# Kernel optimization log

Hardware: AMD Instinct MI355X
Metric: run time of the kernel (lower is better)

Reference implementation:

```python
import jax, jax.numpy as jnp
import numpy as np

B, T, C = 4, 2048, 1024
T_PAST = 2048


def setup_inputs() -> dict:
    key = jax.random.key(0)
    ks = jax.random.split(key, 9)
    s = 1.0 / np.sqrt(C)
    return {
        "x": jax.random.normal(ks[0], (B, T, C), dtype=jnp.float32),
        "past_k": jax.random.normal(ks[1], (B, T_PAST, C), dtype=jnp.float32),
        "past_v": jax.random.normal(ks[2], (B, T_PAST, C), dtype=jnp.float32),
        "Wq": jax.random.normal(ks[3], (C, C), dtype=jnp.float32) * s,
        "bq": jnp.zeros((C,), dtype=jnp.float32),
        "Wk": jax.random.normal(ks[4], (C, C), dtype=jnp.float32) * s,
        "bk": jnp.zeros((C,), dtype=jnp.float32),
        "Wv": jax.random.normal(ks[5], (C, C), dtype=jnp.float32) * s,
        "bv": jnp.zeros((C,), dtype=jnp.float32),
    }


def reference(x, past_k, past_v, Wq, bq, Wk, bk, Wv, bv):
    Bb, Tt, Cc = x.shape
    # nn.Linear: y = x @ W^T + b
    Q = jnp.einsum('btc,dc->btd', x, Wq) + bq
    K = jnp.einsum('btc,dc->btd', x, Wk) + bk
    V = jnp.einsum('btc,dc->btd', x, Wv) + bv
    K = jnp.concatenate([past_k, K], axis=1)
    V = jnp.concatenate([past_v, V], axis=1)
    T_total = K.shape[1]
    scores = jnp.einsum('btc,bsc->bts', Q, K) / jnp.sqrt(jnp.float32(Cc))
    # Faithful to torch.tril(ones(T, T_total)): allow j <= i (even across cache)
    mask = jnp.arange(T_total)[None, :] <= jnp.arange(Tt)[:, None]
    scores = jnp.where(mask[None, :, :], scores, -jnp.inf)
    weights = jax.nn.softmax(scores, axis=-1)
    out = jnp.einsum('bts,bsc->btc', weights, V)
    return (out, K, V)
```

## Files before the change

### kernel.cpp

```cpp
#include <hip/hip_runtime.h>


typedef __bf16 bf16x8 __attribute__((ext_vector_type(8)));
typedef float f32x4 __attribute__((ext_vector_type(4)));

#define BB   4
#define TQ   2048
#define CD   1024
#define TPAST 2048
#define TTOT 4096
#define MROWS (BB * TQ)
#define SSTRIDE_FALLBACK ((size_t)TTOT * CD * 2)
#define SLOTU 8192
#define WSLOT 12288

__device__ __forceinline__ unsigned short f32_to_bf16u(float f) {
  unsigned int u = __float_as_uint(f);
  u += 0x7FFFu + ((u >> 16) & 1u);
  return (unsigned short)(u >> 16);
}
__device__ __forceinline__ float bf16u_to_f32(unsigned short h) {
  unsigned int u = ((unsigned int)h) << 16;
  return __uint_as_float(u);
}
__device__ __forceinline__ unsigned int pack_bf16(float a, float b) {
  return (unsigned int)f32_to_bf16u(a) | ((unsigned int)f32_to_bf16u(b) << 16);
}

__device__ __forceinline__ void gload_lds16(const unsigned short* g,
                                            unsigned short* l) {
  __builtin_amdgcn_global_load_lds(
      (const __attribute__((address_space(1))) void*)g,
      (__attribute__((address_space(3))) void*)l, 16, 0, 0);
}

__device__ __forceinline__ const unsigned short* swz_src(
    const unsigned short* base, size_t rowStart, size_t ld,
    int part, int wv, int lane) {
  int row = part * 64 + wv * 16 + (lane >> 2);
  int gp = (lane & 3) ^ ((lane >> 2) & 3);
  return base + (rowStart + row) * ld + gp * 8;
}

struct StagePtrs { const unsigned short *a0, *a1, *b0, *b1; };

__device__ __forceinline__ void stage_step(StagePtrs& p, unsigned short* lds,
                                           int stOff, int wv) {
  unsigned short* base = lds + stOff + wv * 512;
  gload_lds16(p.a0, base);
  gload_lds16(p.a1, base + 2048);
  gload_lds16(p.b0, base + 4096);
  gload_lds16(p.b1, base + 6144);
  p.a0 += 32; p.a1 += 32; p.b0 += 32; p.b1 += 32;
}

__device__ __forceinline__ void gemm_core_v2(
    StagePtrs p, unsigned short* lds, int NT,
    int wr, int wc, int lane, int wv, f32x4 acc[4][4]) {
  const int gph8 = (((lane >> 4) ^ (lane & 3))) * 8;
  const int aRd = (wr * 64 + (lane & 15)) * 32 + gph8;
  const int bRd = 4096 + (wc * 64 + (lane & 15)) * 32 + gph8;
  stage_step(p, lds, 0, wv);
  stage_step(p, lds, SLOTU, wv);
  int stOff = 2 * SLOTU;
  int rdOff = 0;
  for (int t = 0; t < NT; ++t) {
    if (t + 2 < NT) {
      stage_step(p, lds, stOff, wv);
      stOff = (stOff == 2 * SLOTU) ? 0 : stOff + SLOTU;
    }
    const int rem = NT - 1 - t;
    if (rem >= 2)      asm volatile("s_waitcnt vmcnt(8)" ::: "memory");
    else if (rem == 1) asm volatile("s_waitcnt vmcnt(4)" ::: "memory");
    else               asm volatile("s_waitcnt vmcnt(0)" ::: "memory");
    asm volatile("s_barrier" ::: "memory");
    bf16x8 af[4], bg[4];
#pragma unroll
    for (int i = 0; i < 4; ++i)
      af[i] = *(const bf16x8*)&lds[rdOff + aRd + i * 512];
#pragma unroll
    for (int i = 0; i < 4; ++i)
      bg[i] = *(const bf16x8*)&lds[rdOff + bRd + i * 512];
    asm volatile("s_waitcnt lgkmcnt(0)" ::: "memory");
    __builtin_amdgcn_sched_barrier(0);
    asm volatile("s_barrier" ::: "memory");
    __builtin_amdgcn_s_setprio(1);
#pragma unroll
    for (int mi = 0; mi < 4; ++mi)
#pragma unroll
      for (int ni = 0; ni < 4; ++ni)
        acc[mi][ni] = __builtin_amdgcn_mfma_f32_16x16x32_bf16(
            af[mi], bg[ni], acc[mi][ni], 0, 0, 0);
    __builtin_amdgcn_s_setprio(0);
    rdOff = (rdOff == 2 * SLOTU) ? 0 : rdOff + SLOTU;
  }
}

struct StageW { const unsigned short *a0, *a1, *b0, *b1, *b2, *b3; };

__device__ __forceinline__ void stage_w(StageW& p, unsigned short* lds,
                                        int stOff, int wv) {
  unsigned short* base = lds + stOff + wv * 512;
  gload_lds16(p.a0, base);
  gload_lds16(p.a1, base + 2048);
  gload_lds16(p.b0, base + 4096);
  gload_lds16(p.b1, base + 6144);
  gload_lds16(p.b2, base + 8192);
  gload_lds16(p.b3, base + 10240);
  p.a0 += 32; p.a1 += 32; p.b0 += 32; p.b1 += 32; p.b2 += 32; p.b3 += 32;
}

__device__ __forceinline__ void gemm_core_w(
    StageW p, unsigned short* lds, int NT,
    int wr, int wc, int lane, int wv, f32x4 acc[4][8]) {
  const int gph8 = (((lane >> 4) ^ (lane & 3))) * 8;
  const int aRd = (wr * 64 + (lane & 15)) * 32 + gph8;
  const int bRd = 4096 + (wc * 128 + (lane & 15)) * 32 + gph8;
  stage_w(p, lds, 0, wv);
  int stOff = WSLOT, rdOff = 0;
  for (int t = 0; t < NT; ++t) {
    if (t + 1 < NT) {
      stage_w(p, lds, stOff, wv);
      stOff ^= WSLOT;
    }
    if (t + 1 < NT) asm volatile("s_waitcnt vmcnt(6)" ::: "memory");
    else            asm volatile("s_waitcnt vmcnt(0)" ::: "memory");
    asm volatile("s_barrier" ::: "memory");
    bf16x8 af[4], bg[8];
#pragma unroll
    for (int i = 0; i < 4; ++i)
      af[i] = *(const bf16x8*)&lds[rdOff + aRd + i * 512];
#pragma unroll
    for (int i = 0; i < 8; ++i)
      bg[i] = *(const bf16x8*)&lds[rdOff + bRd + i * 512];
    asm volatile("s_waitcnt lgkmcnt(0)" ::: "memory");
    __builtin_amdgcn_sched_barrier(0);
    asm volatile("s_barrier" ::: "memory");
    __builtin_amdgcn_s_setprio(1);
#pragma unroll
    for (int mi = 0; mi < 4; ++mi)
#pragma unroll
      for (int ni = 0; ni < 8; ++ni)
        acc[mi][ni] = __builtin_amdgcn_mfma_f32_16x16x32_bf16(
            af[mi], bg[ni], acc[mi][ni], 0, 0, 0);
    __builtin_amdgcn_s_setprio(0);
    rdOff ^= WSLOT;
  }
}

#define TP_PAD 134
#define VCT_BLOCKS 2048
#define R0_END 2097152
#define R1_END 2359296
#define R2_END 2621440
#define R3_END 2883584
#define R4_END 4980736
__global__ __launch_bounds__(256) void prep(
    const float* __restrict__ x, const float* __restrict__ wq,
    const float* __restrict__ wk, const float* __restrict__ wv,
    const float* __restrict__ pk, const float* __restrict__ pV,
    unsigned short* __restrict__ xb, unsigned short* __restrict__ wqb,
    unsigned short* __restrict__ wkb, unsigned short* __restrict__ wvb,
    unsigned short* __restrict__ kb,
    float* __restrict__ outV, unsigned short* __restrict__ VT,
    float* __restrict__ outKcopy) {
  const int tid = threadIdx.x;
  if (blockIdx.x < VCT_BLOCKS) {
    __shared__ unsigned short T[32 * TP_PAD];
    const int bid = blockIdx.x;
    const int s0 = (bid & 63) * 32, c0 = ((bid >> 6) & 7) * 128, b = bid >> 9;
    const int s = tid >> 3, i8 = tid & 7;
    const float* src = &pV[(size_t)(b * TPAST + s0 + s) * CD + c0];
    float* dst = &outV[(size_t)b * (TTOT * CD) + (size_t)(s0 + s) * CD + c0];
#pragma unroll
    for (int k = 0; k < 4; ++k) {
      int c = k * 32 + i8 * 4;
      float4 f = *(const float4*)&src[c];
      *(float4*)&dst[c] = f;
      *(unsigned int*)&T[s * TP_PAD + c]     = pack_bf16(f.x, f.y);
      *(unsigned int*)&T[s * TP_PAD + c + 2] = pack_bf16(f.z, f.w);
    }
    __syncthreads();
    const int c = tid >> 2, sq = tid & 3;
#pragma unroll
    for (int ii = 0; ii < 2; ++ii) {
      int cc = c + ii * 64;
      unsigned short tmp[8];
#pragma unroll
      for (int j = 0; j < 8; ++j) tmp[j] = T[(sq * 8 + j) * TP_PAD + cc];
      *(uint4*)&VT[(size_t)(b * CD + c0 + cc) * TPAST + s0 + sq * 8] = *(uint4*)tmp;
    }
    return;
  }
  int i = (blockIdx.x - VCT_BLOCKS) * 256 + tid;
  const float* src; unsigned short* dst; int off;
  bool isPk = false;
  if (i < R0_END)      { src = x;  dst = xb;  off = i; }
  else if (i < R1_END) { src = wq; dst = wqb; off = i - R0_END; }
  else if (i < R2_END) { src = wk; dst = wkb; off = i - R1_END; }
  else if (i < R3_END) { src = wv; dst = wvb; off = i - R2_END; }
  else                 { src = pk; dst = kb;  off = i - R3_END; isPk = true; }
  float4 f = ((const float4*)src)[off];
  uint2 o;
  o.x = pack_bf16(f.x, f.y);
  o.y = pack_bf16(f.z, f.w);
  ((uint2*)dst)[off] = o;
  if (isPk && outKcopy) {
    int b = off >> 19;
    int rem = off & 524287;
    ((float4*)outKcopy)[(size_t)b * 1048576 + rem] = f;
  }
}

__global__ __launch_bounds__(256) void copy_past_kernel(
    const float* __restrict__ src, float* __restrict__ dst) {
  int i = blockIdx.x * 256 + threadIdx.x;
  int b = i >> 19;
  int rem = i & 524287;
  ((float4*)dst)[(size_t)b * 1048576 + rem] = ((const float4*)src)[i];
}

__global__ __launch_bounds__(256, 2) void proj_qkv(
    const unsigned short* __restrict__ A,
    const unsigned short* __restrict__ Wq_,
    const unsigned short* __restrict__ Wv_,
    const unsigned short* __restrict__ Wk_,
    const float* __restrict__ bq_, const float* __restrict__ bv_,
    const float* __restrict__ bk_,
    unsigned short* __restrict__ outQ,
    float* __restrict__ outV, float* __restrict__ outK) {
  __shared__ unsigned short lds[2 * WSLOT];
  const int tm = blockIdx.x * 128;
  const int which = blockIdx.y >> 2;
  const int tn = (blockIdx.y & 3) * 256;
  const unsigned short* W = (which == 0) ? Wq_ : (which == 1) ? Wv_ : Wk_;
  const float* bias = (which == 0) ? bq_ : (which == 1) ? bv_ : bk_;
  const int tid = threadIdx.x, lane = tid & 63, wv = tid >> 6;
  const int wr = wv >> 1, wc = wv & 1;
  StageW p;
  p.a0 = swz_src(A, tm, CD, 0, wv, lane);
  p.a1 = swz_src(A, tm, CD, 1, wv, lane);
  p.b0 = swz_src(W, tn, CD, 0, wv, lane);
  p.b1 = swz_src(W, tn, CD, 1, wv, lane);
  p.b2 = swz_src(W, tn, CD, 2, wv, lane);
  p.b3 = swz_src(W, tn, CD, 3, wv, lane);
  f32x4 acc[4][8] = {};
  gemm_core_w(p, lds, CD / 32, wr, wc, lane, wv, acc);
  const int rsub = (lane >> 4) * 4, csub = lane & 15;
#pragma unroll
  for (int mi = 0; mi < 4; ++mi)
#pragma unroll
    for (int ni = 0; ni < 8; ++ni) {
      int gcn = tn + wc * 128 + ni * 16 + csub;
      float bvv = bias[gcn];
#pragma unroll
      for (int r = 0; r < 4; ++r) {
        int grw = tm + wr * 64 + mi * 16 + rsub + r;
        float v = acc[mi][ni][r] + bvv;
        if (which == 0) {
          outQ[(size_t)grw * CD + gcn] = f32_to_bf16u(v * 0.03125f);
        } else {
          int b = grw >> 11, t = grw & (TQ - 1);
          float* o = (which == 1) ? outV : outK;
          o[(size_t)b * (TTOT * CD) + (size_t)(TPAST + t) * CD + gcn] = v;
        }
      }
    }
}

__global__ __launch_bounds__(256, 3) void score_gemm(
    const unsigned short* __restrict__ Q,
    const unsigned short* __restrict__ KB,
    unsigned short* __restrict__ S16, size_t sstride,
    float* __restrict__ l_part) {
  const int t0 = blockIdx.x * 128, s0 = blockIdx.y * 128, b = blockIdx.z;
  if (s0 > t0) return;
  __shared__ unsigned short lds[3 * SLOTU];
  __shared__ float lpart[128][2];
  const int tid = threadIdx.x, lane = tid & 63, wv = tid >> 6;
  const int wr = wv >> 1, wc = wv & 1;
  StagePtrs p;
  p.a0 = swz_src(Q, (size_t)b * TQ + t0, CD, 0, wv, lane);
  p.a1 = swz_src(Q, (size_t)b * TQ + t0, CD, 1, wv, lane);
  p.b0 = swz_src(KB, (size_t)b * TPAST + s0, CD, 0, wv, lane);
  p.b1 = swz_src(KB, (size_t)b * TPAST + s0, CD, 1, wv, lane);
  f32x4 acc[4][4] = {};
  gemm_core_v2(p, lds, CD / 32, wr, wc, lane, wv, acc);
  const int rsub = (lane >> 4) * 4, csub = lane & 15;
  float rsum[4][4];
#pragma unroll
  for (int mi = 0; mi < 4; ++mi)
#pragma unroll
    for (int r = 0; r < 4; ++r) rsum[mi][r] = 0.f;
#pragma unroll
  for (int mi = 0; mi < 4; ++mi)
#pragma unroll
    for (int ni = 0; ni < 4; ++ni) {
      int gs = s0 + wc * 64 + ni * 16 + csub;
#pragma unroll
      for (int r = 0; r < 4; ++r) {
        int gt = t0 + wr * 64 + mi * 16 + rsub + r;
        float e = (gs <= gt) ? __expf(acc[mi][ni][r] - 16.f) : 0.f;
        unsigned short h = f32_to_bf16u(e);
        S16[(size_t)b * sstride + (size_t)gt * TPAST + gs] = h;
        rsum[mi][r] += bf16u_to_f32(h);
      }
    }
#pragma unroll
  for (int mi = 0; mi < 4; ++mi)
#pragma unroll
    for (int r = 0; r < 4; ++r) {
      float v = rsum[mi][r];
      v += __shfl_xor(v, 1);
      v += __shfl_xor(v, 2);
      v += __shfl_xor(v, 4);
      v += __shfl_xor(v, 8);
      rsum[mi][r] = v;
    }
  if ((lane & 15) == 0) {
#pragma unroll
    for (int mi = 0; mi < 4; ++mi)
#pragma unroll
      for (int r = 0; r < 4; ++r)
        lpart[wr * 64 + mi * 16 + rsub + r][wc] = rsum[mi][r];
  }
  __syncthreads();
  if (tid < 128)
    l_part[((size_t)b * TQ + t0 + tid) * 16 + (s0 >> 7)] =
        lpart[tid][0] + lpart[tid][1];
}

__global__ __launch_bounds__(256, 3) void pv_gemm(
    const unsigned short* __restrict__ Pb,
    const unsigned short* __restrict__ VT,
    float* __restrict__ O, size_t sstride,
    const float* __restrict__ l_part) {
  const int t0 = blockIdx.x * 128, c0 = blockIdx.y * 128, b = blockIdx.z;
  __shared__ unsigned short lds[3 * SLOTU];
  const int tid = threadIdx.x, lane = tid & 63, wv = tid >> 6;
  const int wr = wv >> 1, wc = wv & 1;
  StagePtrs p;
  p.a0 = swz_src(Pb + (size_t)b * sstride, t0, TPAST, 0, wv, lane);
  p.a1 = swz_src(Pb + (size_t)b * sstride, t0, TPAST, 1, wv, lane);
  p.b0 = swz_src(VT, (size_t)b * CD + c0, TPAST, 0, wv, lane);
  p.b1 = swz_src(VT, (size_t)b * CD + c0, TPAST, 1, wv, lane);
  f32x4 acc[4][4] = {};
  const int s_end = (t0 + 128 < TPAST) ? (t0 + 128) : TPAST;
  gemm_core_v2(p, lds, s_end / 32, wr, wc, lane, wv, acc);
  __syncthreads();
  float* linv = (float*)lds;
  if (tid < 128) {
    const float* lp = &l_part[((size_t)b * TQ + t0 + tid) * 16];
    float s = 0.f;
    const int nj = (t0 >> 7) + 1;
    for (int j = 0; j < nj; ++j) s += lp[j];
    linv[tid] = 1.0f / s;
  }
  __syncthreads();
  const int rsub = (lane >> 4) * 4, csub = lane & 15;
#pragma unroll
  for (int mi = 0; mi < 4; ++mi)
#pragma unroll
    for (int ni = 0; ni < 4; ++ni) {
      int gcn = c0 + wc * 64 + ni * 16 + csub;
#pragma unroll
      for (int r = 0; r < 4; ++r) {
        int lrow = wr * 64 + mi * 16 + rsub + r;
        int gt = t0 + lrow;
        O[(size_t)(b * TQ + gt) * CD + gcn] = acc[mi][ni][r] * linv[lrow];
      }
    }
}

extern "C" void kernel_launch(void* const* d_in, const int* in_sizes, int n_in,
                              void* d_out, int out_size, void* d_ws, size_t ws_size,
                              hipStream_t stream) {
  const float* x  = (const float*)d_in[0];
  const float* pk = (const float*)d_in[1];
  const float* pv = (const float*)d_in[2];
  const float* Wq = (const float*)d_in[3];
  const float* bq = (const float*)d_in[4];
  const float* Wk = (const float*)d_in[5];
  const float* bk = (const float*)d_in[6];
  const float* Wv = (const float*)d_in[7];
  const float* bv = (const float*)d_in[8];

  float* out  = (float*)d_out;
  float* outK = out + (size_t)BB * TQ * CD;
  float* outV = outK + (size_t)BB * TTOT * CD;

  unsigned short* xb  = (unsigned short*)d_ws;
  unsigned short* wqb = xb + (size_t)MROWS * CD;
  unsigned short* wkb = wqb + (size_t)CD * CD;
  unsigned short* wvb = wkb + (size_t)CD * CD;
  unsigned short* qb  = wvb + (size_t)CD * CD;
  unsigned short* vtb = qb + (size_t)MROWS * CD;
  unsigned short* kb  = vtb + (size_t)BB * CD * TPAST;
  unsigned short* wsEnd = kb + (size_t)BB * TPAST * CD;

  const size_t baseBytes = (size_t)((char*)wsEnd - (char*)d_ws);
  const size_t s16Bytes  = (size_t)BB * TQ * TPAST * 2;
  const size_t lpBytes   = (size_t)BB * TQ * 16 * 4;
  const bool fit = ws_size >= baseBytes + s16Bytes + lpBytes;

  unsigned short* S16;
  float* l_part;
  size_t sstride;
  if (fit) {
    S16 = wsEnd;
    l_part = (float*)(S16 + (size_t)BB * TQ * TPAST);
    sstride = (size_t)TQ * TPAST;
  } else {
    S16 = (unsigned short*)outK;
    l_part = (float*)wsEnd;
    sstride = SSTRIDE_FALLBACK;
  }

  prep<<<VCT_BLOCKS + R4_END / 256, 256, 0, stream>>>(
      x, Wq, Wk, Wv, pk, pv, xb, wqb, wkb, wvb, kb, outV, vtb,
      fit ? outK : nullptr);
  proj_qkv<<<dim3(MROWS / 128, 12), 256, 0, stream>>>(
      xb, wqb, wvb, wkb, bq, bv, bk, qb, outV, outK);
  score_gemm<<<dim3(TQ / 128, TPAST / 128, BB), 256, 0, stream>>>(
      qb, kb, S16, sstride, l_part);
  pv_gemm<<<dim3(TQ / 128, CD / 128, BB), 256, 0, stream>>>(
      S16, vtb, out, sstride, l_part);
  if (!fit)
    copy_past_kernel<<<BB * TPAST * CD / 4 / 256, 256, 0, stream>>>(pk, outK);
}
```

Before: 211.1 us.

## Retune GEMM pipelines, add nontemporal stores, reverse causal block order

In the projection GEMM, the LDS ring grows from double to triple buffering with a two-tile prefetch depth and matching vmcnt waits. In the score and PV GEMMs, prefetch depth drops to one tile over the three existing slots, which removes the second barrier and the lgkmcnt wait per iteration. Large fp32 output writes (V/K copies, projected K/V, attention output) become nontemporal stores so they do not pollute cache. Score and PV blocks are launched in reverse t order so the heaviest causal tiles are scheduled first. The larger LDS footprint in the projection kernel may reduce occupancy.

```diff
diff --git a/kernel.cpp b/kernel.cpp
--- a/kernel.cpp
+++ b/kernel.cpp
@@ -26,6 +26,11 @@
 __device__ __forceinline__ unsigned int pack_bf16(float a, float b) {
   return (unsigned int)f32_to_bf16u(a) | ((unsigned int)f32_to_bf16u(b) << 16);
 }
+__device__ __forceinline__ void nt_store4(float4 f, float* p) {
+  f32x4 v;
+  v[0] = f.x; v[1] = f.y; v[2] = f.z; v[3] = f.w;
+  __builtin_nontemporal_store(v, (f32x4*)p);
+}
 
 __device__ __forceinline__ void gload_lds16(const unsigned short* g,
                                             unsigned short* l) {
@@ -61,18 +66,16 @@
   const int aRd = (wr * 64 + (lane & 15)) * 32 + gph8;
   const int bRd = 4096 + (wc * 64 + (lane & 15)) * 32 + gph8;
   stage_step(p, lds, 0, wv);
-  stage_step(p, lds, SLOTU, wv);
-  int stOff = 2 * SLOTU;
+  int stOff = SLOTU;
   int rdOff = 0;
   for (int t = 0; t < NT; ++t) {
-    if (t + 2 < NT) {
+    if (t + 1 < NT) {
       stage_step(p, lds, stOff, wv);
       stOff = (stOff == 2 * SLOTU) ? 0 : stOff + SLOTU;
-    }
-    const int rem = NT - 1 - t;
-    if (rem >= 2)      asm volatile("s_waitcnt vmcnt(8)" ::: "memory");
-    else if (rem == 1) asm volatile("s_waitcnt vmcnt(4)" ::: "memory");
-    else               asm volatile("s_waitcnt vmcnt(0)" ::: "memory");
+      asm volatile("s_waitcnt vmcnt(4)" ::: "memory");
+    } else {
+      asm volatile("s_waitcnt vmcnt(0)" ::: "memory");
+    }
     asm volatile("s_barrier" ::: "memory");
     bf16x8 af[4], bg[4];
 #pragma unroll
@@ -81,9 +84,6 @@
 #pragma unroll
     for (int i = 0; i < 4; ++i)
       bg[i] = *(const bf16x8*)&lds[rdOff + bRd + i * 512];
-    asm volatile("s_waitcnt lgkmcnt(0)" ::: "memory");
-    __builtin_amdgcn_sched_barrier(0);
-    asm volatile("s_barrier" ::: "memory");
     __builtin_amdgcn_s_setprio(1);
 #pragma unroll
     for (int mi = 0; mi < 4; ++mi)
@@ -117,14 +117,17 @@
   const int aRd = (wr * 64 + (lane & 15)) * 32 + gph8;
   const int bRd = 4096 + (wc * 128 + (lane & 15)) * 32 + gph8;
   stage_w(p, lds, 0, wv);
-  int stOff = WSLOT, rdOff = 0;
+  stage_w(p, lds, WSLOT, wv);
+  int stOff = 2 * WSLOT, rdOff = 0;
   for (int t = 0; t < NT; ++t) {
-    if (t + 1 < NT) {
+    if (t + 2 < NT) {
       stage_w(p, lds, stOff, wv);
-      stOff ^= WSLOT;
-    }
-    if (t + 1 < NT) asm volatile("s_waitcnt vmcnt(6)" ::: "memory");
-    else            asm volatile("s_waitcnt vmcnt(0)" ::: "memory");
+      stOff = (stOff == 2 * WSLOT) ? 0 : stOff + WSLOT;
+    }
+    const int rem = NT - 1 - t;
+    if (rem >= 2)      asm volatile("s_waitcnt vmcnt(12)" ::: "memory");
+    else if (rem == 1) asm volatile("s_waitcnt vmcnt(6)" ::: "memory");
+    else               asm volatile("s_waitcnt vmcnt(0)" ::: "memory");
     asm volatile("s_barrier" ::: "memory");
     bf16x8 af[4], bg[8];
 #pragma unroll
@@ -144,7 +147,7 @@
         acc[mi][ni] = __builtin_amdgcn_mfma_f32_16x16x32_bf16(
             af[mi], bg[ni], acc[mi][ni], 0, 0, 0);
     __builtin_amdgcn_s_setprio(0);
-    rdOff ^= WSLOT;
+    rdOff = (rdOff == 2 * WSLOT) ? 0 : rdOff + WSLOT;
   }
 }
 
@@ -176,7 +179,7 @@
     for (int k = 0; k < 4; ++k) {
       int c = k * 32 + i8 * 4;
       float4 f = *(const float4*)&src[c];
-      *(float4*)&dst[c] = f;
+      nt_store4(f, &dst[c]);
       *(unsigned int*)&T[s * TP_PAD + c]     = pack_bf16(f.x, f.y);
       *(unsigned int*)&T[s * TP_PAD + c + 2] = pack_bf16(f.z, f.w);
     }
@@ -208,7 +211,7 @@
   if (isPk && outKcopy) {
     int b = off >> 19;
     int rem = off & 524287;
-    ((float4*)outKcopy)[(size_t)b * 1048576 + rem] = f;
+    nt_store4(f, outKcopy + ((size_t)b * 1048576 + rem) * 4);
   }
 }
 
@@ -229,7 +232,7 @@
     const float* __restrict__ bk_,
     unsigned short* __restrict__ outQ,
     float* __restrict__ outV, float* __restrict__ outK) {
-  __shared__ unsigned short lds[2 * WSLOT];
+  __shared__ unsigned short lds[3 * WSLOT];
   const int tm = blockIdx.x * 128;
   const int which = blockIdx.y >> 2;
   const int tn = (blockIdx.y & 3) * 256;
@@ -262,7 +265,8 @@
         } else {
           int b = grw >> 11, t = grw & (TQ - 1);
           float* o = (which == 1) ? outV : outK;
-          o[(size_t)b * (TTOT * CD) + (size_t)(TPAST + t) * CD + gcn] = v;
+          __builtin_nontemporal_store(
+              v, &o[(size_t)b * (TTOT * CD) + (size_t)(TPAST + t) * CD + gcn]);
         }
       }
     }
@@ -273,7 +277,8 @@
     const unsigned short* __restrict__ KB,
     unsigned short* __restrict__ S16, size_t sstride,
     float* __restrict__ l_part) {
-  const int t0 = blockIdx.x * 128, s0 = blockIdx.y * 128, b = blockIdx.z;
+  const int t0 = (TQ / 128 - 1 - blockIdx.x) * 128;
+  const int s0 = blockIdx.y * 128, b = blockIdx.z;
   if (s0 > t0) return;
   __shared__ unsigned short lds[3 * SLOTU];
   __shared__ float lpart[128][2];
@@ -335,7 +340,8 @@
     const unsigned short* __restrict__ VT,
     float* __restrict__ O, size_t sstride,
     const float* __restrict__ l_part) {
-  const int t0 = blockIdx.x * 128, c0 = blockIdx.y * 128, b = blockIdx.z;
+  const int t0 = (TQ / 128 - 1 - blockIdx.x) * 128;
+  const int c0 = blockIdx.y * 128, b = blockIdx.z;
   __shared__ unsigned short lds[3 * SLOTU];
   const int tid = threadIdx.x, lane = tid & 63, wv = tid >> 6;
   const int wr = wv >> 1, wc = wv & 1;
@@ -367,7 +373,8 @@
       for (int r = 0; r < 4; ++r) {
         int lrow = wr * 64 + mi * 16 + rsub + r;
         int gt = t0 + lrow;
-        O[(size_t)(b * TQ + gt) * CD + gcn] = acc[mi][ni][r] * linv[lrow];
+        __builtin_nontemporal_store(
+            acc[mi][ni][r] * linv[lrow], &O[(size_t)(b * TQ + gt) * CD + gcn]);
       }
     }
 }
```

After: 203.7 us. 1.04x faster.
